# Kernel optimization log

Hardware: AMD Instinct MI355X
Metric: run time of the kernel (lower is better)

## Reference

```python
import jax, jax.numpy as jnp
import numpy as np

EPS_SIM = 1e-10
EPS_NORM = 1e-12


def setup_inputs() -> dict:
    key = jax.random.key(0)
    k1, k2, k3, k4, k5 = jax.random.split(key, 5)
    B, CH, H, W = 64, 512, 28, 28
    R = CH // 16  # reduction
    x = jax.random.normal(k1, (B, CH, H, W), dtype=jnp.float32)
    # torch nn.Linear weights are [out, in]
    wD = jax.random.normal(k2, (R, CH), dtype=jnp.float32) * (1.0 / np.sqrt(CH))
    bD = jax.random.normal(k3, (R,), dtype=jnp.float32) * 0.01
    wU = jax.random.normal(k4, (CH, R), dtype=jnp.float32) * (1.0 / np.sqrt(R))
    bU = jax.random.normal(k5, (CH,), dtype=jnp.float32) * 0.01
    return {"x": x, "wD": wD, "bD": bD, "wU": wU, "bU": bU}


def _hybrid_weight(xap):
    # xap: [B, CH, N]; returns row-diag-masked, globally normalized similarity Wij [B, CH, CH]
    gram = jnp.einsum('bin,bjn->bij', xap, xap)           # [B,CH,CH]
    sq = jnp.sum(xap * xap, axis=-1)                      # [B,CH]
    d2 = sq[:, :, None] + sq[:, None, :] - 2.0 * gram
    d = jnp.sqrt(d2)
    d = jnp.where(jnp.isnan(d), 0.0, d)                   # NaN mask (sqrt of negatives)
    d = jnp.maximum(d, 0.0)                               # clamp(0, inf)
    mean_d = jnp.mean(d, axis=(1, 2), keepdims=True)
    l2_sim = jnp.exp(-d / (mean_d + EPS_SIM))
    w = jnp.sqrt(sq)                                      # per-channel L2 norm
    denom = jnp.maximum(w[:, :, None] * w[:, None, :], EPS_SIM)
    cos = gram / denom
    cos = jnp.where(jnp.isnan(cos), 0.0, cos)
    cos = jnp.maximum(cos, 0.0)
    sim = cos * l2_sim
    CH = sim.shape[1]
    sim = sim * (1.0 - jnp.eye(CH, dtype=sim.dtype))      # zero diagonal
    Wij = sim / (jnp.sum(sim, axis=(1, 2), keepdims=True) + EPS_SIM)
    return Wij


def reference(x, wD, bD, wU, bU):
    B, CH, H, W = x.shape
    r = 7  # rdim[512]
    # adaptive avg pool to 7x7 (H, W divisible by 7 -> exact block average)
    xap = x.reshape(B, CH, r, H // r, r, W // r).mean(axis=(3, 5)).reshape(B, CH, r * r)
    Wij = jax.lax.stop_gradient(_hybrid_weight(xap))      # computed under no_grad in torch
    gap = x.mean(axis=(2, 3))                             # [B,CH] global avg pool
    mu = gap.mean(axis=1, keepdims=True)
    std = jnp.std(gap, axis=1, ddof=1, keepdims=True)     # torch std is unbiased
    z = (gap - mu) / std                                  # [B,CH]
    # diag(z z^T Wij)_i = z_i * (z^T Wij)_i  -> avoid materializing zz^T
    local_mi = z * jnp.einsum('bj,bji->bi', z, Wij)       # [B,CH]
    m = local_mi.mean(axis=1, keepdims=True)
    s = jnp.std(local_mi, axis=1, ddof=1, keepdims=True)
    ch = (local_mi - m) / (s + EPS_NORM)                  # normal_G
    h = jax.nn.relu(ch @ wD.T + bD)
    att = h @ wU.T + bU
    scale = jax.nn.sigmoid(att)[:, :, None, None]
    return x * scale
```

## Files before the change

### kernel.cpp

```cpp
#include <hip/hip_runtime.h>
#include <hip/hip_bf16.h>
#include <stdint.h>

#define NB 64
#define NC 512
#define NHW 784
#define NK 49
#define KP 64
#define NR 32
#define NTASK 10

typedef short sh8 __attribute__((ext_vector_type(8)));
typedef float f32x4 __attribute__((ext_vector_type(4)));
typedef int v4i __attribute__((ext_vector_type(4)));

__device__ __forceinline__ float wave_sum(float v) {
#pragma unroll
  for (int o = 32; o; o >>= 1) v += __shfl_xor(v, o);
  return v;
}

__device__ __forceinline__ void task_decode(int s, int& ti, int& tj) {
  if (s < 4) { ti = 0; tj = s; }
  else if (s < 7) { ti = 1; tj = s - 3; }
  else if (s < 9) { ti = 2; tj = s - 5; }
  else { ti = 3; tj = 3; }
}

__global__ __launch_bounds__(256) void pool_kernel(const float* __restrict__ x,
                                                   __hip_bfloat16* __restrict__ xap,
                                                   float* __restrict__ wbuf,
                                                   float* __restrict__ gap) {
  int wid = threadIdx.x >> 6, lane = threadIdx.x & 63;
  int row = blockIdx.x * 4 + wid;
  const float* xr = x + (size_t)row * NHW;
  float bin = 0.f;
  if (lane < NK) {
    int pr = lane / 7, pc = lane - pr * 7;
    const float4* p = (const float4*)(xr + pr * 112 + pc * 4);
    float s = 0.f;
#pragma unroll
    for (int i = 0; i < 4; ++i) {
      float4 v = p[i * 7];
      s += (v.x + v.y) + (v.z + v.w);
    }
    bin = s * 0.0625f;
  }
  float s1 = wave_sum(bin);
  float s2 = wave_sum(bin * bin);
  xap[(size_t)row * KP + lane] = __float2bfloat16(bin);
  if (lane == 0) {
    wbuf[row] = sqrtf(s2);
    gap[row] = s1 * (1.f / 49.f);
  }
}

__global__ __launch_bounds__(256) void meand_kernel(const __hip_bfloat16* __restrict__ xap,
                                                    const float* __restrict__ wbuf,
                                                    float* __restrict__ dpart) {
  __shared__ __align__(16) __hip_bfloat16 Ab[128 * KP];
  __shared__ __align__(16) __hip_bfloat16 Bb[128 * KP];
  __shared__ float wiL[128], wjL[128];
  __shared__ float red[4];
  int blk = blockIdx.x;
  int b = blk / NTASK, s = blk - b * NTASK;
  int ti, tj;
  task_decode(s, ti, tj);
  bool diag = (ti == tj);
  int i0 = ti * 128, j0 = tj * 128;
  int t = threadIdx.x;
  const v4i* ga = (const v4i*)(xap + ((size_t)b * NC + i0) * KP);
  const v4i* gb = (const v4i*)(xap + ((size_t)b * NC + j0) * KP);
  v4i* la = (v4i*)Ab;
  v4i* lb = (v4i*)Bb;
#pragma unroll
  for (int q = 0; q < 4; ++q) {
    int cid = q * 256 + t;
    int r = cid >> 3, c = cid & 7;
    int dst = (r << 3) | (c ^ (r & 7));
    la[dst] = ga[cid];
    lb[dst] = gb[cid];
  }
  if (t < 128) {
    wiL[t] = wbuf[b * NC + i0 + t];
    wjL[t] = wbuf[b * NC + j0 + t];
  }
  __syncthreads();
  int lane = t & 63, wave = t >> 6;
  int wi = wave >> 1, wn = wave & 1;
  int l15 = lane & 15, g16 = lane >> 4;
  sh8 af[4][2], bfr[4][2];
#pragma unroll
  for (int f = 0; f < 4; ++f) {
#pragma unroll
    for (int ks = 0; ks < 2; ++ks) {
      int ra = wi * 64 + f * 16 + l15;
      int rb = wn * 64 + f * 16 + l15;
      int cg = ks * 4 + g16;
      af[f][ks] = __builtin_bit_cast(sh8, ((const v4i*)Ab)[(ra << 3) | (cg ^ (ra & 7))]);
      bfr[f][ks] = __builtin_bit_cast(sh8, ((const v4i*)Bb)[(rb << 3) | (cg ^ (rb & 7))]);
    }
  }
  f32x4 acc[4][4];
#pragma unroll
  for (int fm = 0; fm < 4; ++fm)
#pragma unroll
    for (int fn = 0; fn < 4; ++fn) acc[fm][fn] = (f32x4){0.f, 0.f, 0.f, 0.f};
#pragma unroll
  for (int ks = 0; ks < 2; ++ks)
#pragma unroll
    for (int fm = 0; fm < 4; ++fm)
#pragma unroll
      for (int fn = 0; fn < 4; ++fn)
        acc[fm][fn] =
            __builtin_amdgcn_mfma_f32_16x16x32_bf16(af[fm][ks], bfr[fn][ks], acc[fm][fn], 0, 0, 0);
  float a2[4][4], b2[4];
#pragma unroll
  for (int fm = 0; fm < 4; ++fm)
#pragma unroll
    for (int rg = 0; rg < 4; ++rg) {
      float a = wiL[wi * 64 + fm * 16 + g16 * 4 + rg];
      a2[fm][rg] = a * a;
    }
#pragma unroll
  for (int fn = 0; fn < 4; ++fn) {
    float w = wjL[wn * 64 + fn * 16 + l15];
    b2[fn] = w * w;
  }
  float dsum = 0.f;
#pragma unroll
  for (int fm = 0; fm < 4; ++fm)
#pragma unroll
    for (int fn = 0; fn < 4; ++fn)
#pragma unroll
      for (int rg = 0; rg < 4; ++rg) {
        float d2 = fmaf(-2.f, acc[fm][fn][rg], a2[fm][rg] + b2[fn]);
        dsum += sqrtf(fmaxf(d2, 0.f));
      }
  dsum = wave_sum(dsum);
  if (lane == 0) red[wave] = dsum;
  __syncthreads();
  if (t == 0) dpart[blk] = ((red[0] + red[1]) + (red[2] + red[3])) * (diag ? 1.f : 2.f);
}

__global__ __launch_bounds__(256) void sim_kernel(const __hip_bfloat16* __restrict__ xap,
                                                  const float* __restrict__ wbuf,
                                                  const float* __restrict__ gap,
                                                  const float* __restrict__ dpart,
                                                  float* __restrict__ tpart,
                                                  float* __restrict__ spart) {
  __shared__ __align__(16) __hip_bfloat16 Ab[128 * KP];
  __shared__ __align__(16) __hip_bfloat16 Bb[128 * KP];
  __shared__ float wiL[128], wjL[128], zL[NC], tfull[NC];
  __shared__ float red[4];
  int blk = blockIdx.x;
  int b = blk / NTASK, s = blk - b * NTASK;
  int ti, tj;
  task_decode(s, ti, tj);
  bool diag = (ti == tj);
  int i0 = ti * 128, j0 = tj * 128;
  int t = threadIdx.x;
  int lane = t & 63, wave = t >> 6;
  float dsb = 0.f;
#pragma unroll
  for (int k = 0; k < NTASK; ++k) dsb += dpart[b * NTASK + k];
  float nim = -1.44269504f / (dsb * (1.f / 262144.f) + 1e-10f);
  const v4i* ga = (const v4i*)(xap + ((size_t)b * NC + i0) * KP);
  const v4i* gb = (const v4i*)(xap + ((size_t)b * NC + j0) * KP);
  v4i* la = (v4i*)Ab;
  v4i* lb = (v4i*)Bb;
#pragma unroll
  for (int q = 0; q < 4; ++q) {
    int cid = q * 256 + t;
    int r = cid >> 3, c = cid & 7;
    int dst = (r << 3) | (c ^ (r & 7));
    la[dst] = ga[cid];
    lb[dst] = gb[cid];
  }
  if (t < 128) {
    wiL[t] = wbuf[b * NC + i0 + t];
    wjL[t] = wbuf[b * NC + j0 + t];
  }
  tfull[t] = 0.f;
  tfull[t + 256] = 0.f;
  float g0 = gap[b * NC + t], g1 = gap[b * NC + t + 256];
  float s1 = wave_sum(g0 + g1);
  if (lane == 0) red[wave] = s1;
  __syncthreads();
  float mu = ((red[0] + red[1]) + (red[2] + red[3])) * (1.f / 512.f);
  float e0 = g0 - mu, e1 = g1 - mu;
  __syncthreads();
  float vv = wave_sum(e0 * e0 + e1 * e1);
  if (lane == 0) red[wave] = vv;
  __syncthreads();
  float inv_sd = 1.f / sqrtf(((red[0] + red[1]) + (red[2] + red[3])) * (1.f / 511.f));
  zL[t] = e0 * inv_sd;
  zL[t + 256] = e1 * inv_sd;
  __syncthreads();
  int wi = wave >> 1, wn = wave & 1;
  int l15 = lane & 15, g16 = lane >> 4;
  sh8 af[4][2], bfr[4][2];
#pragma unroll
  for (int f = 0; f < 4; ++f) {
#pragma unroll
    for (int ks = 0; ks < 2; ++ks) {
      int ra = wi * 64 + f * 16 + l15;
      int rb = wn * 64 + f * 16 + l15;
      int cg = ks * 4 + g16;
      af[f][ks] = __builtin_bit_cast(sh8, ((const v4i*)Ab)[(ra << 3) | (cg ^ (ra & 7))]);
      bfr[f][ks] = __builtin_bit_cast(sh8, ((const v4i*)Bb)[(rb << 3) | (cg ^ (rb & 7))]);
    }
  }
  f32x4 acc[4][4];
#pragma unroll
  for (int fm = 0; fm < 4; ++fm)
#pragma unroll
    for (int fn = 0; fn < 4; ++fn) acc[fm][fn] = (f32x4){0.f, 0.f, 0.f, 0.f};
#pragma unroll
  for (int ks = 0; ks < 2; ++ks)
#pragma unroll
    for (int fm = 0; fm < 4; ++fm)
#pragma unroll
      for (int fn = 0; fn < 4; ++fn)
        acc[fm][fn] =
            __builtin_amdgcn_mfma_f32_16x16x32_bf16(af[fm][ks], bfr[fn][ks], acc[fm][fn], 0, 0, 0);
  float a2[4][4], ia[4][4], zi[4][4];
#pragma unroll
  for (int fm = 0; fm < 4; ++fm)
#pragma unroll
    for (int rg = 0; rg < 4; ++rg) {
      int il = wi * 64 + fm * 16 + g16 * 4 + rg;
      float a = wiL[il];
      a2[fm][rg] = a * a;
      ia[fm][rg] = 1.f / fmaxf(a, 1e-7f);
      zi[fm][rg] = zL[i0 + il];
    }
  float b2[4], ib[4], zj[4];
#pragma unroll
  for (int fn = 0; fn < 4; ++fn) {
    int jl = wn * 64 + fn * 16 + l15;
    float w = wjL[jl];
    b2[fn] = w * w;
    ib[fn] = 1.f / fmaxf(w, 1e-7f);
    zj[fn] = zL[j0 + jl];
  }
  float ssum = 0.f;
  float trow[4][4];
  float tcol[4] = {0.f, 0.f, 0.f, 0.f};
#pragma unroll
  for (int fm = 0; fm < 4; ++fm)
#pragma unroll
    for (int rg = 0; rg < 4; ++rg) trow[fm][rg] = 0.f;
#pragma unroll
  for (int fm = 0; fm < 4; ++fm)
#pragma unroll
    for (int fn = 0; fn < 4; ++fn) {
      float ibn = ib[fn];
#pragma unroll
      for (int rg = 0; rg < 4; ++rg) {
        float g = acc[fm][fn][rg];
        float d2 = fmaf(-2.f, g, a2[fm][rg] + b2[fn]);
        float d = sqrtf(fmaxf(d2, 0.f));
        float sim = fmaxf(g, 0.f) * ia[fm][rg] * ibn * exp2f(d * nim);
        if (diag) {
          int il = wi * 64 + fm * 16 + g16 * 4 + rg;
          int jl = wn * 64 + fn * 16 + l15;
          if (il == jl) sim = 0.f;
        }
        ssum += sim;
        trow[fm][rg] = fmaf(sim, zj[fn], trow[fm][rg]);
        tcol[fn] = fmaf(sim, zi[fm][rg], tcol[fn]);
      }
    }
#pragma unroll
  for (int fm = 0; fm < 4; ++fm)
#pragma unroll
    for (int rg = 0; rg < 4; ++rg) {
      float v = trow[fm][rg];
#pragma unroll
      for (int o = 8; o; o >>= 1) v += __shfl_xor(v, o);
      if (l15 == 0) atomicAdd(&tfull[i0 + wi * 64 + fm * 16 + g16 * 4 + rg], v);
    }
  if (!diag) {
#pragma unroll
    for (int fn = 0; fn < 4; ++fn) {
      float v = tcol[fn];
      v += __shfl_xor(v, 16);
      v += __shfl_xor(v, 32);
      if (g16 == 0) atomicAdd(&tfull[j0 + wn * 64 + fn * 16 + l15], v);
    }
  }
  ssum = wave_sum(ssum);
  if (lane == 0) red[wave] = ssum;
  __syncthreads();
  if (t == 0) spart[blk] = ((red[0] + red[1]) + (red[2] + red[3])) * (diag ? 1.f : 2.f);
  tpart[(size_t)blk * NC + t] = tfull[t];
  tpart[(size_t)blk * NC + t + 256] = tfull[t + 256];
}

__global__ __launch_bounds__(256) void mlp_kernel(const float* __restrict__ gap,
                                                  const float* __restrict__ tpart,
                                                  const float* __restrict__ spart,
                                                  const float* __restrict__ wD,
                                                  const float* __restrict__ bD,
                                                  const float* __restrict__ wU,
                                                  const float* __restrict__ bU,
                                                  float* __restrict__ scl) {
  __shared__ float red[4];
  __shared__ float chL[NC];
  __shared__ float hL[NR];
  int b = blockIdx.x, t = threadIdx.x;
  int lane = t & 63, wid = t >> 6;
  float S = 0.f;
#pragma unroll
  for (int k = 0; k < NTASK; ++k) S += spart[b * NTASK + k];
  float invS = 1.f / (S + 1e-10f);
  float t0 = 0.f, t1 = 0.f;
#pragma unroll
  for (int j = 0; j < NTASK; ++j) {
    t0 += tpart[((size_t)b * NTASK + j) * NC + t];
    t1 += tpart[((size_t)b * NTASK + j) * NC + t + 256];
  }
  float g0 = gap[b * NC + t], g1 = gap[b * NC + t + 256];
  float s1 = wave_sum(g0 + g1);
  if (lane == 0) red[wid] = s1;
  __syncthreads();
  float mu = ((red[0] + red[1]) + (red[2] + red[3])) * (1.f / 512.f);
  float e0 = g0 - mu, e1 = g1 - mu;
  __syncthreads();
  float vv = wave_sum(e0 * e0 + e1 * e1);
  if (lane == 0) red[wid] = vv;
  __syncthreads();
  float inv_sd = 1.f / sqrtf(((red[0] + red[1]) + (red[2] + red[3])) * (1.f / 511.f));
  float lm0 = e0 * inv_sd * t0 * invS;
  float lm1 = e1 * inv_sd * t1 * invS;
  __syncthreads();
  float s2 = wave_sum(lm0 + lm1);
  if (lane == 0) red[wid] = s2;
  __syncthreads();
  float m = ((red[0] + red[1]) + (red[2] + red[3])) * (1.f / 512.f);
  float d0 = lm0 - m, d1 = lm1 - m;
  __syncthreads();
  float v2 = wave_sum(d0 * d0 + d1 * d1);
  if (lane == 0) red[wid] = v2;
  __syncthreads();
  float sd = sqrtf(((red[0] + red[1]) + (red[2] + red[3])) * (1.f / 511.f)) + 1e-12f;
  chL[t] = d0 / sd;
  chL[t + 256] = d1 / sd;
  __syncthreads();
  int k = t >> 3, p = t & 7;
  const float* wrow = wD + k * NC + p * 64;
  const float* cp = chL + p * 64;
  float hp = 0.f;
#pragma unroll
  for (int i = 0; i < 64; ++i) hp += wrow[i] * cp[i];
#pragma unroll
  for (int o = 4; o; o >>= 1) hp += __shfl_xor(hp, o);
  if (p == 0) hL[k] = fmaxf(hp + bD[k], 0.f);
  __syncthreads();
#pragma unroll
  for (int u = 0; u < 2; ++u) {
    int c = t + u * 256;
    const float* wrU = wU + c * NR;
    float att = bU[c];
#pragma unroll
    for (int kk = 0; kk < NR; ++kk) att += hL[kk] * wrU[kk];
    scl[b * NC + c] = 1.f / (1.f + __expf(-att));
  }
}

__global__ __launch_bounds__(256) void scale_kernel(const float* __restrict__ x,
                                                    const float* __restrict__ scl,
                                                    float* __restrict__ out) {
  unsigned idx = blockIdx.x * 256u + threadIdx.x;
  unsigned row = idx / 196u;
  float s = scl[row];
  f32x4 v = __builtin_nontemporal_load(((const f32x4*)x) + idx);
  v *= s;
  __builtin_nontemporal_store(v, ((f32x4*)out) + idx);
}

extern "C" void kernel_launch(void* const* d_in, const int* in_sizes, int n_in,
                              void* d_out, int out_size, void* d_ws, size_t ws_size,
                              hipStream_t stream) {
  const float* x = (const float*)d_in[0];
  const float* wD = (const float*)d_in[1];
  const float* bD = (const float*)d_in[2];
  const float* wU = (const float*)d_in[3];
  const float* bU = (const float*)d_in[4];
  float* out = (float*)d_out;
  char* ws = (char*)d_ws;

  __hip_bfloat16* xap = (__hip_bfloat16*)ws;
  float* fbase = (float*)(ws + (size_t)NB * NC * KP * 2);
  float* wbuf = fbase;
  float* gap = wbuf + NB * NC;
  float* dpart = gap + NB * NC;
  float* spart = dpart + NB * NTASK;
  float* tpart = spart + NB * NTASK;
  float* scl = tpart + NB * NTASK * NC;

  hipLaunchKernelGGL(pool_kernel, dim3(NB * NC / 4), dim3(256), 0, stream, x, xap, wbuf, gap);
  hipLaunchKernelGGL(meand_kernel, dim3(NB * NTASK), dim3(256), 0, stream, xap, wbuf, dpart);
  hipLaunchKernelGGL(sim_kernel, dim3(NB * NTASK), dim3(256), 0, stream, xap, wbuf, gap, dpart,
                     tpart, spart);
  hipLaunchKernelGGL(mlp_kernel, dim3(NB), dim3(256), 0, stream, gap, tpart, spart, wD, bD, wU, bU,
                     scl);
  hipLaunchKernelGGL(scale_kernel, dim3(25088), dim3(256), 0, stream, x, scl, out);
}
```

Measured before the change: 95.01 us.

## Fuse all five stages into one cooperative persistent kernel with grid syncs

Replaces the five separate kernel launches with a single cooperative kernel of 512 blocks that runs pooling, mean-distance, similarity, MLP and scaling phases separated by grid.sync. The aim is to remove launch gaps and tail effects between the small stages, and to let the final scale pass re-read x while it may still be in cache (the scale loads are no longer nontemporal). The cost is grid-wide barriers, a fixed 512-block grid for the bandwidth-bound phases, and only 64 blocks doing work in the MLP phase. The old multi-kernel path is kept as a fallback if the cooperative launch fails.

```diff
diff --git a/kernel.cpp b/kernel.cpp
--- a/kernel.cpp
+++ b/kernel.cpp
@@ -1,6 +1,9 @@
 #include <hip/hip_runtime.h>
 #include <hip/hip_bf16.h>
+#include <hip/hip_cooperative_groups.h>
 #include <stdint.h>
+
+namespace cg = cooperative_groups;
 
 #define NB 64
 #define NC 512
@@ -9,6 +12,7 @@
 #define KP 64
 #define NR 32
 #define NTASK 10
+#define MGRID 512
 
 typedef short sh8 __attribute__((ext_vector_type(8)));
 typedef float f32x4 __attribute__((ext_vector_type(4)));
@@ -25,6 +29,352 @@
   else if (s < 7) { ti = 1; tj = s - 3; }
   else if (s < 9) { ti = 2; tj = s - 5; }
   else { ti = 3; tj = 3; }
+}
+
+__global__ __launch_bounds__(256, 2) void mega_kernel(
+    const float* __restrict__ x, __hip_bfloat16* __restrict__ xap,
+    float* __restrict__ wbuf, float* __restrict__ gap, float* __restrict__ dpart,
+    float* __restrict__ spart, float* __restrict__ tpart, float* __restrict__ scl,
+    const float* __restrict__ wD, const float* __restrict__ bD,
+    const float* __restrict__ wU, const float* __restrict__ bU, float* __restrict__ out) {
+  cg::grid_group grid = cg::this_grid();
+  __shared__ __align__(16) __hip_bfloat16 Ab[128 * KP];
+  __shared__ __align__(16) __hip_bfloat16 Bb[128 * KP];
+  __shared__ float wiL[128], wjL[128], zL[NC], tfull[NC];
+  __shared__ float red[4];
+  __shared__ float hL[NR];
+  int t = threadIdx.x;
+  int lane = t & 63, wave = t >> 6;
+  int blk = blockIdx.x;
+
+#pragma unroll 2
+  for (int it = 0; it < 16; ++it) {
+    int row = (it * MGRID + blk) * 4 + wave;
+    const float* xr = x + (size_t)row * NHW;
+    float bin = 0.f;
+    if (lane < NK) {
+      int pr = lane / 7, pc = lane - pr * 7;
+      const float4* p = (const float4*)(xr + pr * 112 + pc * 4);
+      float s = 0.f;
+#pragma unroll
+      for (int i = 0; i < 4; ++i) {
+        float4 v = p[i * 7];
+        s += (v.x + v.y) + (v.z + v.w);
+      }
+      bin = s * 0.0625f;
+    }
+    float s1 = wave_sum(bin);
+    float s2 = wave_sum(bin * bin);
+    xap[(size_t)row * KP + lane] = __float2bfloat16(bin);
+    if (lane == 0) {
+      wbuf[row] = sqrtf(s2);
+      gap[row] = s1 * (1.f / 49.f);
+    }
+  }
+  grid.sync();
+
+  for (int task = blk; task < NB * NTASK; task += MGRID) {
+    int b = task / NTASK, s = task - b * NTASK;
+    int ti, tj;
+    task_decode(s, ti, tj);
+    bool diag = (ti == tj);
+    int i0 = ti * 128, j0 = tj * 128;
+    const v4i* ga = (const v4i*)(xap + ((size_t)b * NC + i0) * KP);
+    const v4i* gb = (const v4i*)(xap + ((size_t)b * NC + j0) * KP);
+    v4i* la = (v4i*)Ab;
+    v4i* lb = (v4i*)Bb;
+    __syncthreads();
+#pragma unroll
+    for (int q = 0; q < 4; ++q) {
+      int cid = q * 256 + t;
+      int r = cid >> 3, c = cid & 7;
+      int dst = (r << 3) | (c ^ (r & 7));
+      la[dst] = ga[cid];
+      lb[dst] = gb[cid];
+    }
+    if (t < 128) {
+      wiL[t] = wbuf[b * NC + i0 + t];
+      wjL[t] = wbuf[b * NC + j0 + t];
+    }
+    __syncthreads();
+    int wi = wave >> 1, wn = wave & 1;
+    int l15 = lane & 15, g16 = lane >> 4;
+    sh8 af[4][2], bfr[4][2];
+#pragma unroll
+    for (int f = 0; f < 4; ++f) {
+#pragma unroll
+      for (int ks = 0; ks < 2; ++ks) {
+        int ra = wi * 64 + f * 16 + l15;
+        int rb = wn * 64 + f * 16 + l15;
+        int cg2 = ks * 4 + g16;
+        af[f][ks] = __builtin_bit_cast(sh8, ((const v4i*)Ab)[(ra << 3) | (cg2 ^ (ra & 7))]);
+        bfr[f][ks] = __builtin_bit_cast(sh8, ((const v4i*)Bb)[(rb << 3) | (cg2 ^ (rb & 7))]);
+      }
+    }
+    f32x4 acc[4][4];
+#pragma unroll
+    for (int fm = 0; fm < 4; ++fm)
+#pragma unroll
+      for (int fn = 0; fn < 4; ++fn) acc[fm][fn] = (f32x4){0.f, 0.f, 0.f, 0.f};
+#pragma unroll
+    for (int ks = 0; ks < 2; ++ks)
+#pragma unroll
+      for (int fm = 0; fm < 4; ++fm)
+#pragma unroll
+        for (int fn = 0; fn < 4; ++fn)
+          acc[fm][fn] = __builtin_amdgcn_mfma_f32_16x16x32_bf16(af[fm][ks], bfr[fn][ks],
+                                                                acc[fm][fn], 0, 0, 0);
+    float a2[4][4], b2[4];
+#pragma unroll
+    for (int fm = 0; fm < 4; ++fm)
+#pragma unroll
+      for (int rg = 0; rg < 4; ++rg) {
+        float a = wiL[wi * 64 + fm * 16 + g16 * 4 + rg];
+        a2[fm][rg] = a * a;
+      }
+#pragma unroll
+    for (int fn = 0; fn < 4; ++fn) {
+      float w = wjL[wn * 64 + fn * 16 + l15];
+      b2[fn] = w * w;
+    }
+    float dsum = 0.f;
+#pragma unroll
+    for (int fm = 0; fm < 4; ++fm)
+#pragma unroll
+      for (int fn = 0; fn < 4; ++fn)
+#pragma unroll
+        for (int rg = 0; rg < 4; ++rg) {
+          float d2 = fmaf(-2.f, acc[fm][fn][rg], a2[fm][rg] + b2[fn]);
+          dsum += sqrtf(fmaxf(d2, 0.f));
+        }
+    dsum = wave_sum(dsum);
+    if (lane == 0) red[wave] = dsum;
+    __syncthreads();
+    if (t == 0) dpart[task] = ((red[0] + red[1]) + (red[2] + red[3])) * (diag ? 1.f : 2.f);
+  }
+  grid.sync();
+
+  for (int task = blk; task < NB * NTASK; task += MGRID) {
+    int b = task / NTASK, s = task - b * NTASK;
+    int ti, tj;
+    task_decode(s, ti, tj);
+    bool diag = (ti == tj);
+    int i0 = ti * 128, j0 = tj * 128;
+    float dsb = 0.f;
+#pragma unroll
+    for (int k = 0; k < NTASK; ++k) dsb += dpart[b * NTASK + k];
+    float nim = -1.44269504f / (dsb * (1.f / 262144.f) + 1e-10f);
+    const v4i* ga = (const v4i*)(xap + ((size_t)b * NC + i0) * KP);
+    const v4i* gb = (const v4i*)(xap + ((size_t)b * NC + j0) * KP);
+    v4i* la = (v4i*)Ab;
+    v4i* lb = (v4i*)Bb;
+    __syncthreads();
+#pragma unroll
+    for (int q = 0; q < 4; ++q) {
+      int cid = q * 256 + t;
+      int r = cid >> 3, c = cid & 7;
+      int dst = (r << 3) | (c ^ (r & 7));
+      la[dst] = ga[cid];
+      lb[dst] = gb[cid];
+    }
+    if (t < 128) {
+      wiL[t] = wbuf[b * NC + i0 + t];
+      wjL[t] = wbuf[b * NC + j0 + t];
+    }
+    tfull[t] = 0.f;
+    tfull[t + 256] = 0.f;
+    float g0 = gap[b * NC + t], g1 = gap[b * NC + t + 256];
+    float s1 = wave_sum(g0 + g1);
+    if (lane == 0) red[wave] = s1;
+    __syncthreads();
+    float mu = ((red[0] + red[1]) + (red[2] + red[3])) * (1.f / 512.f);
+    float e0 = g0 - mu, e1 = g1 - mu;
+    __syncthreads();
+    float vv = wave_sum(e0 * e0 + e1 * e1);
+    if (lane == 0) red[wave] = vv;
+    __syncthreads();
+    float inv_sd = 1.f / sqrtf(((red[0] + red[1]) + (red[2] + red[3])) * (1.f / 511.f));
+    zL[t] = e0 * inv_sd;
+    zL[t + 256] = e1 * inv_sd;
+    __syncthreads();
+    int wi = wave >> 1, wn = wave & 1;
+    int l15 = lane & 15, g16 = lane >> 4;
+    sh8 af[4][2], bfr[4][2];
+#pragma unroll
+    for (int f = 0; f < 4; ++f) {
+#pragma unroll
+      for (int ks = 0; ks < 2; ++ks) {
+        int ra = wi * 64 + f * 16 + l15;
+        int rb = wn * 64 + f * 16 + l15;
+        int cg2 = ks * 4 + g16;
+        af[f][ks] = __builtin_bit_cast(sh8, ((const v4i*)Ab)[(ra << 3) | (cg2 ^ (ra & 7))]);
+        bfr[f][ks] = __builtin_bit_cast(sh8, ((const v4i*)Bb)[(rb << 3) | (cg2 ^ (rb & 7))]);
+      }
+    }
+    f32x4 acc[4][4];
+#pragma unroll
+    for (int fm = 0; fm < 4; ++fm)
+#pragma unroll
+      for (int fn = 0; fn < 4; ++fn) acc[fm][fn] = (f32x4){0.f, 0.f, 0.f, 0.f};
+#pragma unroll
+    for (int ks = 0; ks < 2; ++ks)
+#pragma unroll
+      for (int fm = 0; fm < 4; ++fm)
+#pragma unroll
+        for (int fn = 0; fn < 4; ++fn)
+          acc[fm][fn] = __builtin_amdgcn_mfma_f32_16x16x32_bf16(af[fm][ks], bfr[fn][ks],
+                                                                acc[fm][fn], 0, 0, 0);
+    float a2[4][4], ia[4][4], zi[4][4];
+#pragma unroll
+    for (int fm = 0; fm < 4; ++fm)
+#pragma unroll
+      for (int rg = 0; rg < 4; ++rg) {
+        int il = wi * 64 + fm * 16 + g16 * 4 + rg;
+        float a = wiL[il];
+        a2[fm][rg] = a * a;
+        ia[fm][rg] = 1.f / fmaxf(a, 1e-7f);
+        zi[fm][rg] = zL[i0 + il];
+      }
+    float b2[4], ib[4], zj[4];
+#pragma unroll
+    for (int fn = 0; fn < 4; ++fn) {
+      int jl = wn * 64 + fn * 16 + l15;
+      float w = wjL[jl];
+      b2[fn] = w * w;
+      ib[fn] = 1.f / fmaxf(w, 1e-7f);
+      zj[fn] = zL[j0 + jl];
+    }
+    float ssum = 0.f;
+    float trow[4][4];
+    float tcol[4] = {0.f, 0.f, 0.f, 0.f};
+#pragma unroll
+    for (int fm = 0; fm < 4; ++fm)
+#pragma unroll
+      for (int rg = 0; rg < 4; ++rg) trow[fm][rg] = 0.f;
+#pragma unroll
+    for (int fm = 0; fm < 4; ++fm)
+#pragma unroll
+      for (int fn = 0; fn < 4; ++fn) {
+        float ibn = ib[fn];
+#pragma unroll
+        for (int rg = 0; rg < 4; ++rg) {
+          float g = acc[fm][fn][rg];
+          float d2 = fmaf(-2.f, g, a2[fm][rg] + b2[fn]);
+          float d = sqrtf(fmaxf(d2, 0.f));
+          float sim = fmaxf(g, 0.f) * ia[fm][rg] * ibn * exp2f(d * nim);
+          if (diag) {
+            int il = wi * 64 + fm * 16 + g16 * 4 + rg;
+            int jl = wn * 64 + fn * 16 + l15;
+            if (il == jl) sim = 0.f;
+          }
+          ssum += sim;
+          trow[fm][rg] = fmaf(sim, zj[fn], trow[fm][rg]);
+          tcol[fn] = fmaf(sim, zi[fm][rg], tcol[fn]);
+        }
+      }
+#pragma unroll
+    for (int fm = 0; fm < 4; ++fm)
+#pragma unroll
+      for (int rg = 0; rg < 4; ++rg) {
+        float v = trow[fm][rg];
+#pragma unroll
+        for (int o = 8; o; o >>= 1) v += __shfl_xor(v, o);
+        if (l15 == 0) atomicAdd(&tfull[i0 + wi * 64 + fm * 16 + g16 * 4 + rg], v);
+      }
+    if (!diag) {
+#pragma unroll
+      for (int fn = 0; fn < 4; ++fn) {
+        float v = tcol[fn];
+        v += __shfl_xor(v, 16);
+        v += __shfl_xor(v, 32);
+        if (g16 == 0) atomicAdd(&tfull[j0 + wn * 64 + fn * 16 + l15], v);
+      }
+    }
+    ssum = wave_sum(ssum);
+    if (lane == 0) red[wave] = ssum;
+    __syncthreads();
+    if (t == 0) spart[task] = ((red[0] + red[1]) + (red[2] + red[3])) * (diag ? 1.f : 2.f);
+    tpart[(size_t)task * NC + t] = tfull[t];
+    tpart[(size_t)task * NC + t + 256] = tfull[t + 256];
+  }
+  grid.sync();
+
+  if (blk < NB) {
+    int b = blk;
+    float* chL = tfull;
+    __syncthreads();
+    float S = 0.f;
+#pragma unroll
+    for (int k = 0; k < NTASK; ++k) S += spart[b * NTASK + k];
+    float invS = 1.f / (S + 1e-10f);
+    float t0 = 0.f, t1 = 0.f;
+#pragma unroll
+    for (int j = 0; j < NTASK; ++j) {
+      t0 += tpart[((size_t)b * NTASK + j) * NC + t];
+      t1 += tpart[((size_t)b * NTASK + j) * NC + t + 256];
+    }
+    float g0 = gap[b * NC + t], g1 = gap[b * NC + t + 256];
+    float s1 = wave_sum(g0 + g1);
+    if (lane == 0) red[wave] = s1;
+    __syncthreads();
+    float mu = ((red[0] + red[1]) + (red[2] + red[3])) * (1.f / 512.f);
+    float e0 = g0 - mu, e1 = g1 - mu;
+    __syncthreads();
+    float vv = wave_sum(e0 * e0 + e1 * e1);
+    if (lane == 0) red[wave] = vv;
+    __syncthreads();
+    float inv_sd = 1.f / sqrtf(((red[0] + red[1]) + (red[2] + red[3])) * (1.f / 511.f));
+    float lm0 = e0 * inv_sd * t0 * invS;
+    float lm1 = e1 * inv_sd * t1 * invS;
+    __syncthreads();
+    float s2 = wave_sum(lm0 + lm1);
+    if (lane == 0) red[wave] = s2;
+    __syncthreads();
+    float m = ((red[0] + red[1]) + (red[2] + red[3])) * (1.f / 512.f);
+    float d0 = lm0 - m, d1 = lm1 - m;
+    __syncthreads();
+    float v2 = wave_sum(d0 * d0 + d1 * d1);
+    if (lane == 0) red[wave] = v2;
+    __syncthreads();
+    float sd = sqrtf(((red[0] + red[1]) + (red[2] + red[3])) * (1.f / 511.f)) + 1e-12f;
+    chL[t] = d0 / sd;
+    chL[t + 256] = d1 / sd;
+    __syncthreads();
+    int k = t >> 3, p = t & 7;
+    const float* wrow = wD + k * NC + p * 64;
+    const float* cp = chL + p * 64;
+    float hp = 0.f;
+#pragma unroll
+    for (int i = 0; i < 64; ++i) hp += wrow[i] * cp[i];
+#pragma unroll
+    for (int o = 4; o; o >>= 1) hp += __shfl_xor(hp, o);
+    if (p == 0) hL[k] = fmaxf(hp + bD[k], 0.f);
+    __syncthreads();
+#pragma unroll
+    for (int u = 0; u < 2; ++u) {
+      int c = t + u * 256;
+      const float* wrU = wU + c * NR;
+      float att = bU[c];
+#pragma unroll
+      for (int kk = 0; kk < NR; ++kk) att += hL[kk] * wrU[kk];
+      scl[b * NC + c] = 1.f / (1.f + __expf(-att));
+    }
+  }
+  grid.sync();
+
+  {
+    const f32x4* xv = (const f32x4*)x;
+    f32x4* ov = (f32x4*)out;
+    int base = blk * 256 + t;
+#pragma unroll 7
+    for (int i = 0; i < 49; ++i) {
+      int idx = i * (MGRID * 256) + base;
+      unsigned row = (unsigned)idx / 196u;
+      f32x4 v = xv[idx];
+      v *= scl[row];
+      __builtin_nontemporal_store(v, ov + idx);
+    }
+  }
 }
 
 __global__ __launch_bounds__(256) void pool_kernel(const float* __restrict__ x,
@@ -96,9 +446,9 @@
     for (int ks = 0; ks < 2; ++ks) {
       int ra = wi * 64 + f * 16 + l15;
       int rb = wn * 64 + f * 16 + l15;
-      int cg = ks * 4 + g16;
-      af[f][ks] = __builtin_bit_cast(sh8, ((const v4i*)Ab)[(ra << 3) | (cg ^ (ra & 7))]);
-      bfr[f][ks] = __builtin_bit_cast(sh8, ((const v4i*)Bb)[(rb << 3) | (cg ^ (rb & 7))]);
+      int cg2 = ks * 4 + g16;
+      af[f][ks] = __builtin_bit_cast(sh8, ((const v4i*)Ab)[(ra << 3) | (cg2 ^ (ra & 7))]);
+      bfr[f][ks] = __builtin_bit_cast(sh8, ((const v4i*)Bb)[(rb << 3) | (cg2 ^ (rb & 7))]);
     }
   }
   f32x4 acc[4][4];
@@ -206,9 +556,9 @@
     for (int ks = 0; ks < 2; ++ks) {
       int ra = wi * 64 + f * 16 + l15;
       int rb = wn * 64 + f * 16 + l15;
-      int cg = ks * 4 + g16;
-      af[f][ks] = __builtin_bit_cast(sh8, ((const v4i*)Ab)[(ra << 3) | (cg ^ (ra & 7))]);
-      bfr[f][ks] = __builtin_bit_cast(sh8, ((const v4i*)Bb)[(rb << 3) | (cg ^ (rb & 7))]);
+      int cg2 = ks * 4 + g16;
+      af[f][ks] = __builtin_bit_cast(sh8, ((const v4i*)Ab)[(ra << 3) | (cg2 ^ (ra & 7))]);
+      bfr[f][ks] = __builtin_bit_cast(sh8, ((const v4i*)Bb)[(rb << 3) | (cg2 ^ (rb & 7))]);
     }
   }
   f32x4 acc[4][4];
@@ -375,7 +725,7 @@
   unsigned idx = blockIdx.x * 256u + threadIdx.x;
   unsigned row = idx / 196u;
   float s = scl[row];
-  f32x4 v = __builtin_nontemporal_load(((const f32x4*)x) + idx);
+  f32x4 v = ((const f32x4*)x)[idx];
   v *= s;
   __builtin_nontemporal_store(v, ((f32x4*)out) + idx);
 }
@@ -400,11 +750,19 @@
   float* tpart = spart + NB * NTASK;
   float* scl = tpart + NB * NTASK * NC;
 
-  hipLaunchKernelGGL(pool_kernel, dim3(NB * NC / 4), dim3(256), 0, stream, x, xap, wbuf, gap);
-  hipLaunchKernelGGL(meand_kernel, dim3(NB * NTASK), dim3(256), 0, stream, xap, wbuf, dpart);
-  hipLaunchKernelGGL(sim_kernel, dim3(NB * NTASK), dim3(256), 0, stream, xap, wbuf, gap, dpart,
-                     tpart, spart);
-  hipLaunchKernelGGL(mlp_kernel, dim3(NB), dim3(256), 0, stream, gap, tpart, spart, wD, bD, wU, bU,
-                     scl);
-  hipLaunchKernelGGL(scale_kernel, dim3(25088), dim3(256), 0, stream, x, scl, out);
-}
+  void* args[] = {(void*)&x,     (void*)&xap,   (void*)&wbuf, (void*)&gap, (void*)&dpart,
+                  (void*)&spart, (void*)&tpart, (void*)&scl,  (void*)&wD,  (void*)&bD,
+                  (void*)&wU,    (void*)&bU,    (void*)&out};
+  hipError_t err = hipLaunchCooperativeKernel((void*)mega_kernel, dim3(MGRID), dim3(256), args,
+                                              0, stream);
+  if (err != hipSuccess) {
+    (void)hipGetLastError();
+    hipLaunchKernelGGL(pool_kernel, dim3(NB * NC / 4), dim3(256), 0, stream, x, xap, wbuf, gap);
+    hipLaunchKernelGGL(meand_kernel, dim3(NB * NTASK), dim3(256), 0, stream, xap, wbuf, dpart);
+    hipLaunchKernelGGL(sim_kernel, dim3(NB * NTASK), dim3(256), 0, stream, xap, wbuf, gap, dpart,
+                       tpart, spart);
+    hipLaunchKernelGGL(mlp_kernel, dim3(NB), dim3(256), 0, stream, gap, tpart, spart, wD, bD, wU,
+                       bU, scl);
+    hipLaunchKernelGGL(scale_kernel, dim3(25088), dim3(256), 0, stream, x, scl, out);
+  }
+}
```

Result: slower. 293.1 us (+208.5%).

## Fuse MLP into sim kernel via last-block counter; coalesce pooling loads

Applied to the files above, without the earlier changes.

Removes the separate MLP launch by having the last finishing sim block per batch, detected with an atomic counter and threadfence, run the normalization and MLP, reusing the z values already in shared memory. The pool kernel now reads each row with contiguous float4 loads across lanes and accumulates bins through shared-memory atomics, instead of strided per-bin loads. The scale kernel's load of x becomes a normal cached load so it may hit in cache. This trades one kernel launch and better coalescing for counter atomics, an extra barrier and a serialized tail in the last block of each batch.

```diff
diff --git a/kernel.cpp b/kernel.cpp
--- a/kernel.cpp
+++ b/kernel.cpp
@@ -30,22 +30,32 @@
 __global__ __launch_bounds__(256) void pool_kernel(const float* __restrict__ x,
                                                    __hip_bfloat16* __restrict__ xap,
                                                    float* __restrict__ wbuf,
-                                                   float* __restrict__ gap) {
-  int wid = threadIdx.x >> 6, lane = threadIdx.x & 63;
+                                                   float* __restrict__ gap,
+                                                   int* __restrict__ cnt) {
+  __shared__ float bins[4][64];
+  int t = threadIdx.x, wid = t >> 6, lane = t & 63;
+  if (blockIdx.x == 0 && t < NB) cnt[t] = 0;
   int row = blockIdx.x * 4 + wid;
-  const float* xr = x + (size_t)row * NHW;
-  float bin = 0.f;
-  if (lane < NK) {
-    int pr = lane / 7, pc = lane - pr * 7;
-    const float4* p = (const float4*)(xr + pr * 112 + pc * 4);
-    float s = 0.f;
-#pragma unroll
-    for (int i = 0; i < 4; ++i) {
-      float4 v = p[i * 7];
-      s += (v.x + v.y) + (v.z + v.w);
-    }
-    bin = s * 0.0625f;
-  }
+  const f32x4* xr = (const f32x4*)(x + (size_t)row * NHW);
+  bins[wid][lane] = 0.f;
+  __syncthreads();
+#pragma unroll
+  for (int i = 0; i < 3; ++i) {
+    int f = i * 64 + lane;
+    f32x4 v = xr[f];
+    float s = (v.x + v.y) + (v.z + v.w);
+    int bi = (f / 28) * 7 + f % 7;
+    atomicAdd(&bins[wid][bi], s);
+  }
+  if (lane < 4) {
+    int f = 192 + lane;
+    f32x4 v = xr[f];
+    float s = (v.x + v.y) + (v.z + v.w);
+    int bi = (f / 28) * 7 + f % 7;
+    atomicAdd(&bins[wid][bi], s);
+  }
+  __syncthreads();
+  float bin = bins[wid][lane] * 0.0625f;
   float s1 = wave_sum(bin);
   float s2 = wave_sum(bin * bin);
   xap[(size_t)row * KP + lane] = __float2bfloat16(bin);
@@ -96,9 +106,9 @@
     for (int ks = 0; ks < 2; ++ks) {
       int ra = wi * 64 + f * 16 + l15;
       int rb = wn * 64 + f * 16 + l15;
-      int cg = ks * 4 + g16;
-      af[f][ks] = __builtin_bit_cast(sh8, ((const v4i*)Ab)[(ra << 3) | (cg ^ (ra & 7))]);
-      bfr[f][ks] = __builtin_bit_cast(sh8, ((const v4i*)Bb)[(rb << 3) | (cg ^ (rb & 7))]);
+      int cg2 = ks * 4 + g16;
+      af[f][ks] = __builtin_bit_cast(sh8, ((const v4i*)Ab)[(ra << 3) | (cg2 ^ (ra & 7))]);
+      bfr[f][ks] = __builtin_bit_cast(sh8, ((const v4i*)Bb)[(rb << 3) | (cg2 ^ (rb & 7))]);
     }
   }
   f32x4 acc[4][4];
@@ -148,11 +158,19 @@
                                                   const float* __restrict__ gap,
                                                   const float* __restrict__ dpart,
                                                   float* __restrict__ tpart,
-                                                  float* __restrict__ spart) {
+                                                  float* __restrict__ spart,
+                                                  const float* __restrict__ wD,
+                                                  const float* __restrict__ bD,
+                                                  const float* __restrict__ wU,
+                                                  const float* __restrict__ bU,
+                                                  float* __restrict__ scl,
+                                                  int* __restrict__ cnt) {
   __shared__ __align__(16) __hip_bfloat16 Ab[128 * KP];
   __shared__ __align__(16) __hip_bfloat16 Bb[128 * KP];
   __shared__ float wiL[128], wjL[128], zL[NC], tfull[NC];
   __shared__ float red[4];
+  __shared__ float hL[NR];
+  __shared__ int lastFlag;
   int blk = blockIdx.x;
   int b = blk / NTASK, s = blk - b * NTASK;
   int ti, tj;
@@ -206,9 +224,9 @@
     for (int ks = 0; ks < 2; ++ks) {
       int ra = wi * 64 + f * 16 + l15;
       int rb = wn * 64 + f * 16 + l15;
-      int cg = ks * 4 + g16;
-      af[f][ks] = __builtin_bit_cast(sh8, ((const v4i*)Ab)[(ra << 3) | (cg ^ (ra & 7))]);
-      bfr[f][ks] = __builtin_bit_cast(sh8, ((const v4i*)Bb)[(rb << 3) | (cg ^ (rb & 7))]);
+      int cg2 = ks * 4 + g16;
+      af[f][ks] = __builtin_bit_cast(sh8, ((const v4i*)Ab)[(ra << 3) | (cg2 ^ (ra & 7))]);
+      bfr[f][ks] = __builtin_bit_cast(sh8, ((const v4i*)Bb)[(rb << 3) | (cg2 ^ (rb & 7))]);
     }
   }
   f32x4 acc[4][4];
@@ -296,21 +314,16 @@
   if (t == 0) spart[blk] = ((red[0] + red[1]) + (red[2] + red[3])) * (diag ? 1.f : 2.f);
   tpart[(size_t)blk * NC + t] = tfull[t];
   tpart[(size_t)blk * NC + t + 256] = tfull[t + 256];
-}
-
-__global__ __launch_bounds__(256) void mlp_kernel(const float* __restrict__ gap,
-                                                  const float* __restrict__ tpart,
-                                                  const float* __restrict__ spart,
-                                                  const float* __restrict__ wD,
-                                                  const float* __restrict__ bD,
-                                                  const float* __restrict__ wU,
-                                                  const float* __restrict__ bU,
-                                                  float* __restrict__ scl) {
-  __shared__ float red[4];
-  __shared__ float chL[NC];
-  __shared__ float hL[NR];
-  int b = blockIdx.x, t = threadIdx.x;
-  int lane = t & 63, wid = t >> 6;
+
+  __threadfence();
+  if (t == 0) {
+    int old = atomicAdd(&cnt[b], 1);
+    lastFlag = (old == NTASK - 1);
+  }
+  __syncthreads();
+  if (!lastFlag) return;
+  __threadfence();
+  float* chL = tfull;
   float S = 0.f;
 #pragma unroll
   for (int k = 0; k < NTASK; ++k) S += spart[b * NTASK + k];
@@ -321,28 +334,17 @@
     t0 += tpart[((size_t)b * NTASK + j) * NC + t];
     t1 += tpart[((size_t)b * NTASK + j) * NC + t + 256];
   }
-  float g0 = gap[b * NC + t], g1 = gap[b * NC + t + 256];
-  float s1 = wave_sum(g0 + g1);
-  if (lane == 0) red[wid] = s1;
-  __syncthreads();
-  float mu = ((red[0] + red[1]) + (red[2] + red[3])) * (1.f / 512.f);
-  float e0 = g0 - mu, e1 = g1 - mu;
-  __syncthreads();
-  float vv = wave_sum(e0 * e0 + e1 * e1);
-  if (lane == 0) red[wid] = vv;
-  __syncthreads();
-  float inv_sd = 1.f / sqrtf(((red[0] + red[1]) + (red[2] + red[3])) * (1.f / 511.f));
-  float lm0 = e0 * inv_sd * t0 * invS;
-  float lm1 = e1 * inv_sd * t1 * invS;
-  __syncthreads();
-  float s2 = wave_sum(lm0 + lm1);
-  if (lane == 0) red[wid] = s2;
+  float lm0 = zL[t] * t0 * invS;
+  float lm1 = zL[t + 256] * t1 * invS;
+  __syncthreads();
+  float q3 = wave_sum(lm0 + lm1);
+  if (lane == 0) red[wave] = q3;
   __syncthreads();
   float m = ((red[0] + red[1]) + (red[2] + red[3])) * (1.f / 512.f);
   float d0 = lm0 - m, d1 = lm1 - m;
   __syncthreads();
-  float v2 = wave_sum(d0 * d0 + d1 * d1);
-  if (lane == 0) red[wid] = v2;
+  float q4 = wave_sum(d0 * d0 + d1 * d1);
+  if (lane == 0) red[wave] = q4;
   __syncthreads();
   float sd = sqrtf(((red[0] + red[1]) + (red[2] + red[3])) * (1.f / 511.f)) + 1e-12f;
   chL[t] = d0 / sd;
@@ -375,7 +377,7 @@
   unsigned idx = blockIdx.x * 256u + threadIdx.x;
   unsigned row = idx / 196u;
   float s = scl[row];
-  f32x4 v = __builtin_nontemporal_load(((const f32x4*)x) + idx);
+  f32x4 v = ((const f32x4*)x)[idx];
   v *= s;
   __builtin_nontemporal_store(v, ((f32x4*)out) + idx);
 }
@@ -399,12 +401,11 @@
   float* spart = dpart + NB * NTASK;
   float* tpart = spart + NB * NTASK;
   float* scl = tpart + NB * NTASK * NC;
-
-  hipLaunchKernelGGL(pool_kernel, dim3(NB * NC / 4), dim3(256), 0, stream, x, xap, wbuf, gap);
+  int* cnt = (int*)(scl + NB * NC);
+
+  hipLaunchKernelGGL(pool_kernel, dim3(NB * NC / 4), dim3(256), 0, stream, x, xap, wbuf, gap, cnt);
   hipLaunchKernelGGL(meand_kernel, dim3(NB * NTASK), dim3(256), 0, stream, xap, wbuf, dpart);
   hipLaunchKernelGGL(sim_kernel, dim3(NB * NTASK), dim3(256), 0, stream, xap, wbuf, gap, dpart,
-                     tpart, spart);
-  hipLaunchKernelGGL(mlp_kernel, dim3(NB), dim3(256), 0, stream, gap, tpart, spart, wD, bD, wU, bU,
-                     scl);
+                     tpart, spart, wD, bD, wU, bU, scl, cnt);
   hipLaunchKernelGGL(scale_kernel, dim3(25088), dim3(256), 0, stream, x, scl, out);
 }
```

Result: slower. 192.1 us (+102.2%).
